# Kernel optimization log

Hardware: AMD Instinct MI355X
Metric: run time of the kernel (lower is better)

The kernel has to match this reference:

```python
import jax, jax.numpy as jnp
import numpy as np

ALPHA = 0.25
GAMMA = 2.0
EDGE_W = 1.0
NODE_W = 1.0

N = 200_000
E = 12_800_000
N_GRAPHS = 16
N_INST = 1000


def setup_inputs() -> dict:
    key = jax.random.key(0)
    k1, k2, k3, k4, k5 = jax.random.split(key, 5)
    edge_logits = jax.random.normal(k1, (E,), dtype=jnp.float32)
    node_logits = jax.random.normal(k2, (N,), dtype=jnp.float32)
    batch = jnp.sort(jax.random.randint(k3, (N,), 0, N_GRAPHS, dtype=jnp.int64) if jax.config.read('jax_enable_x64') else jax.random.randint(k3, (N,), 0, N_GRAPHS, dtype=jnp.int32))
    point_instances = jax.random.randint(k4, (N,), 0, N_INST, dtype=jnp.int32)
    edge_index = jax.random.randint(k5, (2, E), 0, N, dtype=jnp.int32)
    return {"edge_logits": edge_logits, "node_logits": node_logits,
            "batch": batch, "point_instances": point_instances,
            "edge_index": edge_index}


def _bce_with_logits(x, t):
    # numerically stable elementwise BCE-with-logits (reduction='none')
    return jnp.maximum(x, 0.0) - x * t + jnp.log1p(jnp.exp(-jnp.abs(x)))


def _sigmoid_focal_loss(x, t, alpha, gamma):
    # torchvision.ops.sigmoid_focal_loss, reduction='mean'
    p = jax.nn.sigmoid(x)
    ce = _bce_with_logits(x, t)
    p_t = p * t + (1.0 - p) * (1.0 - t)
    loss = ce * (1.0 - p_t) ** gamma
    alpha_t = alpha * t + (1.0 - alpha) * (1.0 - t)
    return jnp.mean(alpha_t * loss)


def _accuracy(x, t):
    # sigmoid > 0.5 -> 1 else 0 (note: == 0.5 maps to 0, as in the original)
    pred = (jax.nn.sigmoid(x) > 0.5).astype(x.dtype)
    return jnp.mean((pred == t).astype(jnp.float32))


def reference(edge_logits, node_logits, batch, point_instances, edge_index):
    src, dst = edge_index[0], edge_index[1]
    pi_s = point_instances[src]
    pi_d = point_instances[dst]
    # edge-wise equivalent of the original N x N mask gathered at edge_index:
    # same instance AND same graph AND both instances nonzero
    same = (pi_s == pi_d) & (batch[src] == batch[dst]) & (pi_s != 0) & (pi_d != 0)
    edge_targets = same.astype(jnp.float32)  # [E]

    edge_loss = _sigmoid_focal_loss(edge_logits, edge_targets, ALPHA, GAMMA)
    edge_acc = _accuracy(edge_logits, edge_targets)

    node_targets = (point_instances != 0).astype(jnp.float32)  # [N]
    node_loss = _sigmoid_focal_loss(node_logits, node_targets, ALPHA, GAMMA)
    node_acc = _accuracy(node_logits, node_targets)

    loss = EDGE_W * edge_loss + NODE_W * node_loss
    return loss, edge_loss, node_loss, edge_acc, node_acc
```

## Files before the change

### kernel.cpp

```cpp
#include <hip/hip_runtime.h>
#include <limits.h>


typedef int   iv4 __attribute__((ext_vector_type(4)));
typedef float fv4 __attribute__((ext_vector_type(4)));

#define MAX_PART 4096

__device__ __forceinline__ float focal_term(float x, int t) {
    float y = t ? -x : x;
    float e = __expf(-fabsf(y));
    float ce = fmaxf(y, 0.f) + __logf(1.f + e);
    float inv = __builtin_amdgcn_rcpf(1.f + e);
    float sg = (y >= 0.f) ? inv : e * inv;
    float w = t ? 0.25f : 0.75f;
    return w * ce * sg * sg;
}

__device__ __forceinline__ float acc_term(float x, int t) {
    return ((x > 0.f) == (t != 0)) ? 1.f : 0.f;
}

__device__ __forceinline__ void block_store4(float v0, float v1, float v2,
                                             float v3, float4* part) {
#pragma unroll
    for (int off = 32; off > 0; off >>= 1) {
        v0 += __shfl_down(v0, off, 64);
        v1 += __shfl_down(v1, off, 64);
        v2 += __shfl_down(v2, off, 64);
        v3 += __shfl_down(v3, off, 64);
    }
    __shared__ float s[4][8];
    int wave = threadIdx.x >> 6;
    int lane = threadIdx.x & 63;
    if (lane == 0) { s[0][wave] = v0; s[1][wave] = v1;
                     s[2][wave] = v2; s[3][wave] = v3; }
    __syncthreads();
    if (threadIdx.x == 0) {
        int nw = blockDim.x >> 6;
        float t0 = 0.f, t1 = 0.f, t2 = 0.f, t3 = 0.f;
        for (int w = 0; w < nw; ++w) {
            t0 += s[0][w]; t1 += s[1][w]; t2 += s[2][w]; t3 += s[3][w];
        }
        part[blockIdx.x] = make_float4(t0, t1, t2, t3);
    }
}

__global__ void __launch_bounds__(256, 4)
fused_kernel(const float* __restrict__ nl,
             const int* __restrict__ batch,
             const int* __restrict__ pi,
             int N,
             const float* __restrict__ el,
             const int* __restrict__ src,
             const int* __restrict__ dst,
             int E, float gscale,
             float4* __restrict__ part) {
    __shared__ int bnd[17];
    if (threadIdx.x < 17) {
        int k = threadIdx.x;
        int lo = 0, hi = N;
        while (lo < hi) {
            int mid = (lo + hi) >> 1;
            if (batch[mid] < k) lo = mid + 1; else hi = mid;
        }
        bnd[k] = lo;
    }
    __syncthreads();

    int tid = blockIdx.x * blockDim.x + threadIdx.x;
    int nth = gridDim.x * blockDim.x;
    int lane = threadIdx.x & 63;
    int wid = tid >> 6;
    int nwaves = nth >> 6;
    float nls = 0.f, nac = 0.f, els = 0.f, eac = 0.f;

    int C = N >> 3;
    const iv4* pi4 = reinterpret_cast<const iv4*>(pi);
    const fv4* nl4 = reinterpret_cast<const fv4*>(nl);
    for (int c = tid; c < C; c += nth) {
        iv4 p0 = pi4[(c << 1) + 0], p1 = pi4[(c << 1) + 1];
        fv4 x0 = nl4[(c << 1) + 0], x1 = nl4[(c << 1) + 1];
        int pv[8] = {p0.x, p0.y, p0.z, p0.w, p1.x, p1.y, p1.z, p1.w};
        float xv[8] = {x0.x, x0.y, x0.z, x0.w, x1.x, x1.y, x1.z, x1.w};
#pragma unroll
        for (int j = 0; j < 8; ++j) {
            int t = (pv[j] != 0) ? 1 : 0;
            nls += focal_term(xv[j], t);
            nac += acc_term(xv[j], t);
        }
    }
    if (tid == 0) {
        for (int i = C << 3; i < N; ++i) {
            int t = (pi[i] != 0) ? 1 : 0;
            float x = nl[i];
            nls += focal_term(x, t);
            nac += acc_term(x, t);
        }
    }

    int NW = E >> 10;
    const fv4* el4 = reinterpret_cast<const fv4*>(el);
    for (int w = wid; w < NW; w += nwaves) {
        int base4 = w << 8;
#pragma unroll
        for (int j = 0; j < 4; ++j) {
            fv4 x = __builtin_nontemporal_load(el4 + base4 + (j << 6) + lane);
            els += focal_term(x.x, 0) + focal_term(x.y, 0) +
                   focal_term(x.z, 0) + focal_term(x.w, 0);
            eac += acc_term(x.x, 0) + acc_term(x.y, 0) +
                   acc_term(x.z, 0) + acc_term(x.w, 0);
        }
    }
    if (tid == 0) {
        for (int i = NW << 10; i < E; ++i) {
            float x = el[i];
            els += focal_term(x, 0);
            eac += acc_term(x, 0);
        }
    }

    const iv4* src4 = reinterpret_cast<const iv4*>(src);
    const iv4* dst4 = reinterpret_cast<const iv4*>(dst);
    for (int w = wid; w < NW; w += nwaves) {
        int base4 = w << 8;
        int si[16], di[16];
#pragma unroll
        for (int j = 0; j < 4; ++j) {
            iv4 s = __builtin_nontemporal_load(src4 + base4 + (j << 6) + lane);
            si[j * 4 + 0] = s.x; si[j * 4 + 1] = s.y;
            si[j * 4 + 2] = s.z; si[j * 4 + 3] = s.w;
        }
#pragma unroll
        for (int j = 0; j < 4; ++j) {
            iv4 d = __builtin_nontemporal_load(dst4 + base4 + (j << 6) + lane);
            di[j * 4 + 0] = d.x; di[j * 4 + 1] = d.y;
            di[j * 4 + 2] = d.z; di[j * 4 + 3] = d.w;
        }
        unsigned int sameM = 0;
#pragma unroll
        for (int i = 0; i < 16; ++i) {
            int s = si[i], d = di[i];
            int gg = (int)((float)s * gscale);
            gg = gg < 0 ? 0 : (gg > 15 ? 15 : gg);
            int lo = bnd[gg], hi = bnd[gg + 1];
            while (s < lo) { --gg; hi = lo; lo = bnd[gg]; }
            while (s >= hi) { ++gg; lo = hi; hi = bnd[gg + 1]; }
            sameM |= (unsigned int)((d >= lo) & (d < hi)) << i;
        }
        while (sameM) {
            int i = (int)__builtin_ctz(sameM);
            sameM &= sameM - 1;
            int s = si[i], d = di[i];
            int ps = pi[s];
            int pd = pi[d];
            if ((ps == pd) & (ps != 0)) {
                int ei = (w << 10) + ((((i >> 2) << 6) + lane) << 2) + (i & 3);
                float x = el[ei];
                els += focal_term(x, 1) - focal_term(x, 0);
                eac += (x > 0.f) ? 1.f : -1.f;
            }
        }
    }
    if (tid == 0) {
        for (int i = NW << 10; i < E; ++i) {
            int s = src[i], d = dst[i];
            int gg = (int)((float)s * gscale);
            gg = gg < 0 ? 0 : (gg > 15 ? 15 : gg);
            int lo = bnd[gg], hi = bnd[gg + 1];
            while (s < lo) { --gg; hi = lo; lo = bnd[gg]; }
            while (s >= hi) { ++gg; lo = hi; hi = bnd[gg + 1]; }
            if ((d >= lo) & (d < hi)) {
                int ps = pi[s], pd = pi[d];
                if ((ps == pd) & (ps != 0)) {
                    float x = el[i];
                    els += focal_term(x, 1) - focal_term(x, 0);
                    eac += (x > 0.f) ? 1.f : -1.f;
                }
            }
        }
    }

    block_store4(nls, nac, els, eac, part);
}

__global__ void node_atomic_kernel(const float* __restrict__ nl,
                                   const int* __restrict__ pi,
                                   int N, float* __restrict__ acc) {
    int stride = gridDim.x * blockDim.x;
    float ls = 0.f, ac = 0.f;
    for (int i = blockIdx.x * blockDim.x + threadIdx.x; i < N; i += stride) {
        int t = (pi[i] != 0) ? 1 : 0;
        float x = nl[i];
        ls += focal_term(x, t);
        ac += acc_term(x, t);
    }
#pragma unroll
    for (int off = 32; off > 0; off >>= 1) {
        ls += __shfl_down(ls, off, 64);
        ac += __shfl_down(ac, off, 64);
    }
    if ((threadIdx.x & 63) == 0) {
        atomicAdd(acc + 2, ls);
        atomicAdd(acc + 3, ac);
    }
}

__global__ void edge_kernel_direct(const float* __restrict__ el,
                                   const int* __restrict__ src,
                                   const int* __restrict__ dst,
                                   const int* __restrict__ batch,
                                   const int* __restrict__ pi,
                                   int E, float* __restrict__ acc) {
    int stride = gridDim.x * blockDim.x;
    float ls = 0.f, ac = 0.f;
    for (int i = blockIdx.x * blockDim.x + threadIdx.x; i < E; i += stride) {
        int ps = pi[src[i]], pd = pi[dst[i]];
        int t = (ps == pd) & (batch[src[i]] == batch[dst[i]]) & (ps != 0);
        float x = el[i];
        ls += focal_term(x, t);
        ac += acc_term(x, t);
    }
#pragma unroll
    for (int off = 32; off > 0; off >>= 1) {
        ls += __shfl_down(ls, off, 64);
        ac += __shfl_down(ac, off, 64);
    }
    if ((threadIdx.x & 63) == 0) {
        atomicAdd(acc + 0, ls);
        atomicAdd(acc + 1, ac);
    }
}

__global__ void finalize_kernel(const float* __restrict__ acc,
                                const float4* __restrict__ p1, int n1,
                                int use_part,
                                float* __restrict__ out, int E, int N) {
    if (use_part) {
        float nls = 0.f, nac = 0.f, els = 0.f, eac = 0.f;
        for (int i = threadIdx.x; i < n1; i += 256) {
            float4 p = p1[i];
            nls += p.x; nac += p.y; els += p.z; eac += p.w;
        }
#pragma unroll
        for (int off = 32; off > 0; off >>= 1) {
            nls += __shfl_down(nls, off, 64);
            nac += __shfl_down(nac, off, 64);
            els += __shfl_down(els, off, 64);
            eac += __shfl_down(eac, off, 64);
        }
        __shared__ float s[4][4];
        int wave = threadIdx.x >> 6;
        int lane = threadIdx.x & 63;
        if (lane == 0) { s[0][wave] = nls; s[1][wave] = nac;
                         s[2][wave] = els; s[3][wave] = eac; }
        __syncthreads();
        if (threadIdx.x == 0) {
            nls = 0.f; nac = 0.f; els = 0.f; eac = 0.f;
            for (int w = 0; w < 4; ++w) {
                nls += s[0][w]; nac += s[1][w];
                els += s[2][w]; eac += s[3][w];
            }
            float invE = 1.f / (float)E;
            float invN = 1.f / (float)N;
            float elm = els * invE, eam = eac * invE;
            float nlm = nls * invN, nam = nac * invN;
            out[0] = elm + nlm;
            out[1] = elm;
            out[2] = nlm;
            out[3] = eam;
            out[4] = nam;
        }
    } else if (threadIdx.x == 0) {
        float invE = 1.f / (float)E;
        float invN = 1.f / (float)N;
        float elm = acc[0] * invE;
        float eam = acc[1] * invE;
        float nlm = acc[2] * invN;
        float nam = acc[3] * invN;
        out[0] = elm + nlm;
        out[1] = elm;
        out[2] = nlm;
        out[3] = eam;
        out[4] = nam;
    }
}

extern "C" void kernel_launch(void* const* d_in, const int* in_sizes, int n_in,
                              void* d_out, int out_size, void* d_ws, size_t ws_size,
                              hipStream_t stream) {
    const float* edge_logits = (const float*)d_in[0];
    const float* node_logits = (const float*)d_in[1];
    const int*   batch       = (const int*)d_in[2];
    const int*   pinst       = (const int*)d_in[3];
    const int*   eidx        = (const int*)d_in[4];
    const int E = in_sizes[0];
    const int N = in_sizes[1];
    const int* src = eidx;
    const int* dst = eidx + E;
    float* out = (float*)d_out;

    float* acc = (float*)d_ws;
    float4* part = (float4*)((char*)d_ws + 256);
    size_t need_full = 256 + MAX_PART * sizeof(float4);

    const bool full = (ws_size >= need_full);
    const int block = 256;

    if (full) {
        int g = 2048;
        if (g > MAX_PART) g = MAX_PART;
        float gscale = 16.0f / (float)N;
        fused_kernel<<<g, block, 0, stream>>>(node_logits, batch, pinst, N,
                                              edge_logits, src, dst, E,
                                              gscale, part);
        finalize_kernel<<<1, 256, 0, stream>>>(acc, part, g, 1, out, E, N);
    } else {
        (void)hipMemsetAsync(d_ws, 0, 16, stream);
        int ng = (N + block - 1) / block;
        if (ng > 2048) ng = 2048;
        node_atomic_kernel<<<ng, block, 0, stream>>>(node_logits, pinst, N, acc);
        int eg = (E + block - 1) / block;
        if (eg > 2048) eg = 2048;
        edge_kernel_direct<<<eg, block, 0, stream>>>(edge_logits, src, dst,
                                                     batch, pinst, E, acc);
        finalize_kernel<<<1, 256, 0, stream>>>(acc, nullptr, 0, 0, out, E, N);
    }
}
```

Before: 200.8 us.

## Fuse edge-logit streaming pass into src/dst pass and size grid to work

Merges the separate edge-logit pass into the src/dst index pass, so each wave loads logits, src and dst for the same 1024-edge chunk in one loop iteration and issues all loads before computing. This gives more memory-level parallelism per iteration and drops a second loop over the edge chunks. The grid size now follows the work, one block per four 1024-edge chunks (3125 blocks at default sizes), capped at MAX_PART, in place of a fixed 2048 blocks. In exchange, more values are live per iteration, which raises register pressure and may lower occupancy.

```diff
diff --git a/kernel.cpp b/kernel.cpp
--- a/kernel.cpp
+++ b/kernel.cpp
@@ -100,30 +100,15 @@
     }
 
     int NW = E >> 10;
-    const fv4* el4 = reinterpret_cast<const fv4*>(el);
-    for (int w = wid; w < NW; w += nwaves) {
-        int base4 = w << 8;
-#pragma unroll
-        for (int j = 0; j < 4; ++j) {
-            fv4 x = __builtin_nontemporal_load(el4 + base4 + (j << 6) + lane);
-            els += focal_term(x.x, 0) + focal_term(x.y, 0) +
-                   focal_term(x.z, 0) + focal_term(x.w, 0);
-            eac += acc_term(x.x, 0) + acc_term(x.y, 0) +
-                   acc_term(x.z, 0) + acc_term(x.w, 0);
-        }
-    }
-    if (tid == 0) {
-        for (int i = NW << 10; i < E; ++i) {
-            float x = el[i];
-            els += focal_term(x, 0);
-            eac += acc_term(x, 0);
-        }
-    }
-
+    const fv4* el4  = reinterpret_cast<const fv4*>(el);
     const iv4* src4 = reinterpret_cast<const iv4*>(src);
     const iv4* dst4 = reinterpret_cast<const iv4*>(dst);
     for (int w = wid; w < NW; w += nwaves) {
         int base4 = w << 8;
+        fv4 x0 = __builtin_nontemporal_load(el4 + base4 + (0 << 6) + lane);
+        fv4 x1 = __builtin_nontemporal_load(el4 + base4 + (1 << 6) + lane);
+        fv4 x2 = __builtin_nontemporal_load(el4 + base4 + (2 << 6) + lane);
+        fv4 x3 = __builtin_nontemporal_load(el4 + base4 + (3 << 6) + lane);
         int si[16], di[16];
 #pragma unroll
         for (int j = 0; j < 4; ++j) {
@@ -137,6 +122,22 @@
             di[j * 4 + 0] = d.x; di[j * 4 + 1] = d.y;
             di[j * 4 + 2] = d.z; di[j * 4 + 3] = d.w;
         }
+        els += focal_term(x0.x, 0) + focal_term(x0.y, 0) +
+               focal_term(x0.z, 0) + focal_term(x0.w, 0) +
+               focal_term(x1.x, 0) + focal_term(x1.y, 0) +
+               focal_term(x1.z, 0) + focal_term(x1.w, 0) +
+               focal_term(x2.x, 0) + focal_term(x2.y, 0) +
+               focal_term(x2.z, 0) + focal_term(x2.w, 0) +
+               focal_term(x3.x, 0) + focal_term(x3.y, 0) +
+               focal_term(x3.z, 0) + focal_term(x3.w, 0);
+        eac += acc_term(x0.x, 0) + acc_term(x0.y, 0) +
+               acc_term(x0.z, 0) + acc_term(x0.w, 0) +
+               acc_term(x1.x, 0) + acc_term(x1.y, 0) +
+               acc_term(x1.z, 0) + acc_term(x1.w, 0) +
+               acc_term(x2.x, 0) + acc_term(x2.y, 0) +
+               acc_term(x2.z, 0) + acc_term(x2.w, 0) +
+               acc_term(x3.x, 0) + acc_term(x3.y, 0) +
+               acc_term(x3.z, 0) + acc_term(x3.w, 0);
         unsigned int sameM = 0;
 #pragma unroll
         for (int i = 0; i < 16; ++i) {
@@ -164,20 +165,20 @@
     }
     if (tid == 0) {
         for (int i = NW << 10; i < E; ++i) {
+            float x = el[i];
             int s = src[i], d = dst[i];
             int gg = (int)((float)s * gscale);
             gg = gg < 0 ? 0 : (gg > 15 ? 15 : gg);
             int lo = bnd[gg], hi = bnd[gg + 1];
             while (s < lo) { --gg; hi = lo; lo = bnd[gg]; }
             while (s >= hi) { ++gg; lo = hi; hi = bnd[gg + 1]; }
+            int t = 0;
             if ((d >= lo) & (d < hi)) {
                 int ps = pi[s], pd = pi[d];
-                if ((ps == pd) & (ps != 0)) {
-                    float x = el[i];
-                    els += focal_term(x, 1) - focal_term(x, 0);
-                    eac += (x > 0.f) ? 1.f : -1.f;
-                }
+                t = (ps == pd) & (ps != 0);
             }
+            els += focal_term(x, t);
+            eac += acc_term(x, t);
         }
     }
 
@@ -308,7 +309,11 @@
     const int block = 256;
 
     if (full) {
-        int g = 2048;
+        int NW = E >> 10;
+        int g = (NW + 3) >> 2;
+        int gn = ((N >> 3) + block - 1) / block;
+        if (gn > g) g = gn;
+        if (g < 1) g = 1;
         if (g > MAX_PART) g = MAX_PART;
         float gscale = 16.0f / (float)N;
         fused_kernel<<<g, block, 0, stream>>>(node_logits, batch, pinst, N,
```

After: 207.1 us. 3.2% more time.
